# Kernel optimization log

Hardware: AMD Instinct MI355X
Metric: run time of the kernel (lower is better)

Reference implementation:

```python
import jax, jax.numpy as jnp
import numpy as np

N = 100_000          # nodes
E = 1_600_000        # real edges (self-loops appended after)
HID = 32             # hidden_dim
RES = 5              # PersistenceImager resolution -> 5x5 image
SIGMA = 0.2          # gaussian bandwidth of persistence image kernel
PRELU_A = 0.1        # F.prelu weight used in the source


def _linear_init(k, fan_in, fan_out):
    k1, k2 = jax.random.split(k)
    s = 1.0 / np.sqrt(fan_in)
    W = jax.random.uniform(k1, (fan_in, fan_out), minval=-s, maxval=s, dtype=jnp.float32)
    b = jax.random.uniform(k2, (fan_out,), minval=-s, maxval=s, dtype=jnp.float32)
    return W, b


def setup_inputs() -> dict:
    key = jax.random.key(0)
    ks = jax.random.split(key, 10)
    # edge list: E random edges, then N self-loops appended at the END
    src = jax.random.randint(ks[0], (E,), 0, N)
    dst = jax.random.randint(ks[1], (E,), 0, N)
    loops = jnp.arange(N)
    edge_index0 = jnp.stack([jnp.concatenate([src, loops]),
                             jnp.concatenate([dst, loops])]).astype(jnp.int64)
    x0 = jax.random.normal(ks[2], (N, 1), dtype=jnp.float32)
    # GIN conv MLPs (Base_Model with out_dim=hidden_dim)
    W1, b1 = _linear_init(ks[3], 1, HID)
    W2, b2 = _linear_init(ks[4], HID, HID)
    W4, b4 = _linear_init(ks[5], HID, HID)
    W3, b3 = _linear_init(ks[6], HID, HID)   # conv3: Linear only, no ReLU
    W5, b5 = _linear_init(ks[7], 2 * HID, HID)  # lin5
    W6, b6 = _linear_init(ks[8], HID, 2)        # lin6
    return dict(x0=x0, edge_index0=edge_index0,
                W1=W1, b1=b1, W2=W2, b2=b2, W4=W4, b4=b4, W3=W3, b3=b3,
                W5=W5, b5=b5, W6=W6, b6=b6)


def _gin_agg(x, src, dst):
    # PyG GINConv with eps=0: (1+eps)*x + sum_{j->i} x_j  (aggregation over the
    # provided edge_index, which here already includes appended self-loops)
    return x + jax.ops.segment_sum(x[src], dst, num_segments=N)


def _prelu(x):
    return jnp.where(x >= 0, x, PRELU_A * x)


def _pers_image(pd):
    # Persistence image on a RESxRES grid over [0,1]^2 of (birth, persistence),
    # gaussian kernel integrated per pixel via normal CDFs, linear pers weight.
    b = pd[:, 0]
    pers = pd[:, 1] - pd[:, 0]
    edges = jnp.linspace(0.0, 1.0, RES + 1)
    inv = 1.0 / (SIGMA * np.sqrt(2.0))
    cdf_b = 0.5 * (1.0 + jax.lax.erf((edges[None, :] - b[:, None]) * inv))   # [E, RES+1]
    cdf_p = 0.5 * (1.0 + jax.lax.erf((edges[None, :] - pers[:, None]) * inv))
    db = cdf_b[:, 1:] - cdf_b[:, :-1]   # [E, RES]
    dp = cdf_p[:, 1:] - cdf_p[:, :-1]
    img = jnp.einsum('e,ei,ej->ij', pers, db, dp)
    return img.reshape(-1)  # [25]


def reference(x0, edge_index0, W1, b1, W2, b2, W4, b4, W3, b3, W5, b5, W6, b6):
    src, dst = edge_index0[0], edge_index0[1]
    # Base_Model GIN path (dropout is identity in eval mode); order 1,2,4,3
    x = jax.nn.relu(_gin_agg(x0, src, dst) @ W1 + b1)
    x = jax.nn.relu(_gin_agg(x, src, dst) @ W2 + b2)
    x = jax.nn.relu(_gin_agg(x, src, dst) @ W4 + b4)
    x = _gin_agg(x, src, dst) @ W3 + b3      # conv3: Linear, no ReLU
    # edge head over the E real edges (drop trailing N self-loops)
    x_in = x[src[:E]]
    x_out = x[dst[:E]]
    h = _prelu(jnp.concatenate([x_in, x_out], axis=-1) @ W5 + b5)
    pd = h @ W6 + b6                          # predicted PD, [E, 2]
    img = _pers_image(pd)                     # persistence image, [25]
    return pd, img
```

## Files before the change

kernel.cpp:

```cpp
#include <hip/hip_runtime.h>
#include <hip/hip_bf16.h>
#include <hip/hip_fp16.h>
#include <math.h>

#define NN 100000
#define EE 1600000
#define ET 1700000
#define HID 32

#define BKT_SHIFT 10
#define BKT_MASK 1023
#define NBKT 98
#define CAP 18944
#define EPB 4096
#define NBLK_A 416
#define NBI 1024

__global__ __launch_bounds__(128) void k_seed(int* __restrict__ bucket_fill) {
    int t = threadIdx.x;
    if (t < NBKT) bucket_fill[t] = t * CAP;
}

__global__ __launch_bounds__(256) void k_bkt_scatter(const int* __restrict__ src32, const int* __restrict__ dst32,
                                                     int* __restrict__ bucket_fill, int2* __restrict__ pairs) {
    __shared__ int h[NBKT];
    __shared__ int bbase[NBKT];
    for (int i = threadIdx.x; i < NBKT; i += 256) h[i] = 0;
    __syncthreads();
    int base = blockIdx.x * EPB;
    for (int k = 0; k < EPB; k += 256) {
        int t = base + k + threadIdx.x;
        if (t < ET) atomicAdd(&h[dst32[t] >> BKT_SHIFT], 1);
    }
    __syncthreads();
    for (int i = threadIdx.x; i < NBKT; i += 256) {
        int c = h[i];
        bbase[i] = c ? atomicAdd(&bucket_fill[i], c) : 0;
        h[i] = 0;
    }
    __syncthreads();
    for (int k = 0; k < EPB; k += 256) {
        int t = base + k + threadIdx.x;
        if (t < ET) {
            int sv = src32[t], dv = dst32[t];
            int b = dv >> BKT_SHIFT;
            int off = atomicAdd(&h[b], 1);
            pairs[bbase[b] + off] = make_int2(sv, dv);
        }
    }
}

__global__ __launch_bounds__(512) void k_bkt_csr(const int2* __restrict__ pairs, const int* __restrict__ bucket_fill,
                                                 int* __restrict__ rowptr, int* __restrict__ rowend,
                                                 int* __restrict__ src_sorted) {
    __shared__ int h[1024];
    __shared__ int tmp[512];
    int t = threadIdx.x;
    int b = blockIdx.x;
    int e0 = b * CAP, e1 = bucket_fill[b];
    int node0 = b << BKT_SHIFT;

    h[t] = 0;
    h[t + 512] = 0;
    __syncthreads();
    for (int e = e0 + t; e < e1; e += 512) atomicAdd(&h[pairs[e].y & BKT_MASK], 1);
    __syncthreads();

    int i0 = 2 * t, i1 = 2 * t + 1;
    int v0 = h[i0], v1 = h[i1];
    int s = v0 + v1;
    tmp[t] = s;
    for (int off = 1; off < 512; off <<= 1) {
        __syncthreads();
        int u = (t >= off) ? tmp[t - off] : 0;
        __syncthreads();
        tmp[t] += u;
    }
    __syncthreads();
    int excl = tmp[t] - s;
    h[i0] = excl;
    h[i1] = excl + v0;
    __syncthreads();

    int n0 = node0 + i0, n1 = node0 + i1;
    if (n0 < NN) { rowptr[n0] = e0 + excl;      rowend[n0] = e0 + excl + v0; }
    if (n1 < NN) { rowptr[n1] = e0 + excl + v0; rowend[n1] = e0 + excl + v0 + v1; }
    __syncthreads();

    for (int e = e0 + t; e < e1; e += 512) {
        int2 p = pairs[e];
        int sl = atomicAdd(&h[p.y & BKT_MASK], 1);
        src_sorted[e0 + sl] = p.x;
    }
}

__device__ __forceinline__ void acc8(uint4 r, float* c) {
    float2 f0 = __half22float2(*reinterpret_cast<__half2*>(&r.x));
    float2 f1 = __half22float2(*reinterpret_cast<__half2*>(&r.y));
    float2 f2 = __half22float2(*reinterpret_cast<__half2*>(&r.z));
    float2 f3 = __half22float2(*reinterpret_cast<__half2*>(&r.w));
    c[0] += f0.x; c[1] += f0.y; c[2] += f1.x; c[3] += f1.y;
    c[4] += f2.x; c[5] += f2.y; c[6] += f3.x; c[7] += f3.y;
}

__global__ __launch_bounds__(256) void k_pull1(const int* __restrict__ rowptr, const int* __restrict__ rowend,
                                               const int* __restrict__ src_sorted,
                                               const float* __restrict__ x0, const float* __restrict__ W1,
                                               const float* __restrict__ b1, __half* __restrict__ hout) {
    __shared__ float W1l[32], b1l[32];
    if (threadIdx.x < 32) {
        W1l[threadIdx.x] = W1[threadIdx.x];
        b1l[threadIdx.x] = b1[threadIdx.x];
    }
    __syncthreads();
    int g = blockIdx.x * 256 + threadIdx.x;
    if (g >= NN) return;
    int e0 = rowptr[g], e1 = rowend[g];
    float a0 = x0[g], a1 = 0.f, a2 = 0.f, a3 = 0.f, a4 = 0.f, a5 = 0.f, a6 = 0.f, a7 = 0.f;
    int e = e0;
    for (; e + 8 <= e1; e += 8) {
        a0 += x0[src_sorted[e + 0]];
        a1 += x0[src_sorted[e + 1]];
        a2 += x0[src_sorted[e + 2]];
        a3 += x0[src_sorted[e + 3]];
        a4 += x0[src_sorted[e + 4]];
        a5 += x0[src_sorted[e + 5]];
        a6 += x0[src_sorted[e + 6]];
        a7 += x0[src_sorted[e + 7]];
    }
    for (; e < e1; ++e) a0 += x0[src_sorted[e]];
    float s = ((a0 + a1) + (a2 + a3)) + ((a4 + a5) + (a6 + a7));

    uint4* orow = reinterpret_cast<uint4*>(hout) + ((size_t)g << 2);
#pragma unroll
    for (int q = 0; q < 4; ++q) {
        float o0 = fmaxf(fmaf(s, W1l[8 * q + 0], b1l[8 * q + 0]), 0.f);
        float o1 = fmaxf(fmaf(s, W1l[8 * q + 1], b1l[8 * q + 1]), 0.f);
        float o2 = fmaxf(fmaf(s, W1l[8 * q + 2], b1l[8 * q + 2]), 0.f);
        float o3 = fmaxf(fmaf(s, W1l[8 * q + 3], b1l[8 * q + 3]), 0.f);
        float o4 = fmaxf(fmaf(s, W1l[8 * q + 4], b1l[8 * q + 4]), 0.f);
        float o5 = fmaxf(fmaf(s, W1l[8 * q + 5], b1l[8 * q + 5]), 0.f);
        float o6 = fmaxf(fmaf(s, W1l[8 * q + 6], b1l[8 * q + 6]), 0.f);
        float o7 = fmaxf(fmaf(s, W1l[8 * q + 7], b1l[8 * q + 7]), 0.f);
        __half2 p0 = __floats2half2_rn(o0, o1);
        __half2 p1 = __floats2half2_rn(o2, o3);
        __half2 p2 = __floats2half2_rn(o4, o5);
        __half2 p3 = __floats2half2_rn(o6, o7);
        orow[q] = make_uint4(*reinterpret_cast<unsigned*>(&p0), *reinterpret_cast<unsigned*>(&p1),
                             *reinterpret_cast<unsigned*>(&p2), *reinterpret_cast<unsigned*>(&p3));
    }
}

template <int RELU>
__global__ __launch_bounds__(256) void k_agg_mm(const int* __restrict__ rowptr, const int* __restrict__ rowend,
                                                const int* __restrict__ src_sorted,
                                                const __half* __restrict__ hin, const float* __restrict__ W,
                                                const float* __restrict__ b, __half* __restrict__ hout) {
    __shared__ float Wl[1024];
    for (int i = threadIdx.x; i < 1024; i += 256) Wl[i] = W[i];
    __syncthreads();
    int g = (blockIdx.x * 256 + threadIdx.x) >> 2;
    if (g >= NN) return;
    int j = threadIdx.x & 3;
    const uint4* tab = reinterpret_cast<const uint4*>(hin);
    int e0 = rowptr[g], e1 = rowend[g];
    float x[8], y[8];
#pragma unroll
    for (int i = 0; i < 8; ++i) { x[i] = 0.f; y[i] = 0.f; }
    acc8(tab[(g << 2) + j], x);
    int e = e0;
    for (; e + 8 <= e1; e += 8) {
        int s0 = src_sorted[e + 0], s1 = src_sorted[e + 1], s2 = src_sorted[e + 2], s3 = src_sorted[e + 3];
        int s4 = src_sorted[e + 4], s5 = src_sorted[e + 5], s6 = src_sorted[e + 6], s7 = src_sorted[e + 7];
        uint4 r0 = tab[(s0 << 2) + j];
        uint4 r1 = tab[(s1 << 2) + j];
        uint4 r2 = tab[(s2 << 2) + j];
        uint4 r3 = tab[(s3 << 2) + j];
        uint4 r4 = tab[(s4 << 2) + j];
        uint4 r5 = tab[(s5 << 2) + j];
        uint4 r6 = tab[(s6 << 2) + j];
        uint4 r7 = tab[(s7 << 2) + j];
        acc8(r0, x); acc8(r1, y); acc8(r2, x); acc8(r3, y);
        acc8(r4, x); acc8(r5, y); acc8(r6, x); acc8(r7, y);
    }
    for (; e < e1; ++e) acc8(tab[(src_sorted[e] << 2) + j], x);
#pragma unroll
    for (int i = 0; i < 8; ++i) x[i] += y[i];

    float o[8];
#pragma unroll
    for (int i = 0; i < 8; ++i) o[i] = b[8 * j + i];
#pragma unroll
    for (int sl = 0; sl < 4; ++sl) {
#pragma unroll
        for (int r = 0; r < 8; ++r) {
            float xk = __shfl(x[r], sl, 4);
            int k = 8 * sl + r;
            float4 w0 = *reinterpret_cast<const float4*>(&Wl[k * 32 + 8 * j]);
            float4 w1 = *reinterpret_cast<const float4*>(&Wl[k * 32 + 8 * j + 4]);
            o[0] = fmaf(xk, w0.x, o[0]); o[1] = fmaf(xk, w0.y, o[1]);
            o[2] = fmaf(xk, w0.z, o[2]); o[3] = fmaf(xk, w0.w, o[3]);
            o[4] = fmaf(xk, w1.x, o[4]); o[5] = fmaf(xk, w1.y, o[5]);
            o[6] = fmaf(xk, w1.z, o[6]); o[7] = fmaf(xk, w1.w, o[7]);
        }
    }
    if (RELU) {
#pragma unroll
        for (int i = 0; i < 8; ++i) o[i] = fmaxf(o[i], 0.f);
    }
    __half2 p0 = __floats2half2_rn(o[0], o[1]);
    __half2 p1 = __floats2half2_rn(o[2], o[3]);
    __half2 p2 = __floats2half2_rn(o[4], o[5]);
    __half2 p3 = __floats2half2_rn(o[6], o[7]);
    uint4 st = make_uint4(*reinterpret_cast<unsigned*>(&p0), *reinterpret_cast<unsigned*>(&p1),
                          *reinterpret_cast<unsigned*>(&p2), *reinterpret_cast<unsigned*>(&p3));
    reinterpret_cast<uint4*>(hout)[(g << 2) + j] = st;
}

__global__ __launch_bounds__(256) void k_agg_mm_proj(const int* __restrict__ rowptr, const int* __restrict__ rowend,
                                                     const int* __restrict__ src_sorted,
                                                     const __half* __restrict__ hin, const float* __restrict__ W3,
                                                     const float* __restrict__ b3,
                                                     const float* __restrict__ W5, const float* __restrict__ b5,
                                                     __half* __restrict__ u16, __half* __restrict__ v16) {
    __shared__ float W3l[1024];
    __shared__ float W5l[2048];
    for (int i = threadIdx.x; i < 1024; i += 256) W3l[i] = W3[i];
    for (int i = threadIdx.x; i < 2048; i += 256) W5l[i] = W5[i];
    __syncthreads();
    int g = (blockIdx.x * 256 + threadIdx.x) >> 2;
    if (g >= NN) return;
    int j = threadIdx.x & 3;
    const uint4* tab = reinterpret_cast<const uint4*>(hin);
    int e0 = rowptr[g], e1 = rowend[g];
    float x[8], y[8];
#pragma unroll
    for (int i = 0; i < 8; ++i) { x[i] = 0.f; y[i] = 0.f; }
    acc8(tab[(g << 2) + j], x);
    int e = e0;
    for (; e + 8 <= e1; e += 8) {
        int s0 = src_sorted[e + 0], s1 = src_sorted[e + 1], s2 = src_sorted[e + 2], s3 = src_sorted[e + 3];
        int s4 = src_sorted[e + 4], s5 = src_sorted[e + 5], s6 = src_sorted[e + 6], s7 = src_sorted[e + 7];
        uint4 r0 = tab[(s0 << 2) + j];
        uint4 r1 = tab[(s1 << 2) + j];
        uint4 r2 = tab[(s2 << 2) + j];
        uint4 r3 = tab[(s3 << 2) + j];
        uint4 r4 = tab[(s4 << 2) + j];
        uint4 r5 = tab[(s5 << 2) + j];
        uint4 r6 = tab[(s6 << 2) + j];
        uint4 r7 = tab[(s7 << 2) + j];
        acc8(r0, x); acc8(r1, y); acc8(r2, x); acc8(r3, y);
        acc8(r4, x); acc8(r5, y); acc8(r6, x); acc8(r7, y);
    }
    for (; e < e1; ++e) acc8(tab[(src_sorted[e] << 2) + j], x);
#pragma unroll
    for (int i = 0; i < 8; ++i) x[i] += y[i];

    float o[8];
#pragma unroll
    for (int i = 0; i < 8; ++i) o[i] = b3[8 * j + i];
#pragma unroll
    for (int sl = 0; sl < 4; ++sl) {
#pragma unroll
        for (int r = 0; r < 8; ++r) {
            float xk = __shfl(x[r], sl, 4);
            int k = 8 * sl + r;
            float4 w0 = *reinterpret_cast<const float4*>(&W3l[k * 32 + 8 * j]);
            float4 w1 = *reinterpret_cast<const float4*>(&W3l[k * 32 + 8 * j + 4]);
            o[0] = fmaf(xk, w0.x, o[0]); o[1] = fmaf(xk, w0.y, o[1]);
            o[2] = fmaf(xk, w0.z, o[2]); o[3] = fmaf(xk, w0.w, o[3]);
            o[4] = fmaf(xk, w1.x, o[4]); o[5] = fmaf(xk, w1.y, o[5]);
            o[6] = fmaf(xk, w1.z, o[6]); o[7] = fmaf(xk, w1.w, o[7]);
        }
    }
    float u[8], v[8];
#pragma unroll
    for (int i = 0; i < 8; ++i) { u[i] = b5[8 * j + i]; v[i] = 0.f; }
#pragma unroll
    for (int sl = 0; sl < 4; ++sl) {
#pragma unroll
        for (int r = 0; r < 8; ++r) {
            float xk = __shfl(o[r], sl, 4);
            int k = 8 * sl + r;
            float4 a0 = *reinterpret_cast<const float4*>(&W5l[k * 32 + 8 * j]);
            float4 a1 = *reinterpret_cast<const float4*>(&W5l[k * 32 + 8 * j + 4]);
            u[0] = fmaf(xk, a0.x, u[0]); u[1] = fmaf(xk, a0.y, u[1]);
            u[2] = fmaf(xk, a0.z, u[2]); u[3] = fmaf(xk, a0.w, u[3]);
            u[4] = fmaf(xk, a1.x, u[4]); u[5] = fmaf(xk, a1.y, u[5]);
            u[6] = fmaf(xk, a1.z, u[6]); u[7] = fmaf(xk, a1.w, u[7]);
            float4 c0 = *reinterpret_cast<const float4*>(&W5l[(32 + k) * 32 + 8 * j]);
            float4 c1 = *reinterpret_cast<const float4*>(&W5l[(32 + k) * 32 + 8 * j + 4]);
            v[0] = fmaf(xk, c0.x, v[0]); v[1] = fmaf(xk, c0.y, v[1]);
            v[2] = fmaf(xk, c0.z, v[2]); v[3] = fmaf(xk, c0.w, v[3]);
            v[4] = fmaf(xk, c1.x, v[4]); v[5] = fmaf(xk, c1.y, v[5]);
            v[6] = fmaf(xk, c1.z, v[6]); v[7] = fmaf(xk, c1.w, v[7]);
        }
    }
    __half2 pu0 = __floats2half2_rn(u[0], u[1]);
    __half2 pu1 = __floats2half2_rn(u[2], u[3]);
    __half2 pu2 = __floats2half2_rn(u[4], u[5]);
    __half2 pu3 = __floats2half2_rn(u[6], u[7]);
    uint4 su = make_uint4(*reinterpret_cast<unsigned*>(&pu0), *reinterpret_cast<unsigned*>(&pu1),
                          *reinterpret_cast<unsigned*>(&pu2), *reinterpret_cast<unsigned*>(&pu3));
    reinterpret_cast<uint4*>(u16)[(g << 2) + j] = su;
    __half2 pv0 = __floats2half2_rn(v[0], v[1]);
    __half2 pv1 = __floats2half2_rn(v[2], v[3]);
    __half2 pv2 = __floats2half2_rn(v[4], v[5]);
    __half2 pv3 = __floats2half2_rn(v[6], v[7]);
    uint4 sv = make_uint4(*reinterpret_cast<unsigned*>(&pv0), *reinterpret_cast<unsigned*>(&pv1),
                          *reinterpret_cast<unsigned*>(&pv2), *reinterpret_cast<unsigned*>(&pv3));
    reinterpret_cast<uint4*>(v16)[(g << 2) + j] = sv;
}

__global__ __launch_bounds__(256) void k_edge(const int* __restrict__ src32, const int* __restrict__ dst32,
                                              const __half* __restrict__ u16, const __half* __restrict__ v16,
                                              const float* __restrict__ W6, const float* __restrict__ b6,
                                              float* __restrict__ pd_out) {
    int ea = blockIdx.x * 512 + threadIdx.x;
    int eb = ea + 256;
    int sa = src32[ea], da = dst32[ea];
    int sb = src32[eb], db = dst32[eb];
    const uint4* pua = reinterpret_cast<const uint4*>(u16 + ((size_t)sa << 5));
    const uint4* pva = reinterpret_cast<const uint4*>(v16 + ((size_t)da << 5));
    const uint4* pub = reinterpret_cast<const uint4*>(u16 + ((size_t)sb << 5));
    const uint4* pvb = reinterpret_cast<const uint4*>(v16 + ((size_t)db << 5));

    uint4 A[4], B[4], C[4], D[4];
#pragma unroll
    for (int q = 0; q < 4; ++q) A[q] = pua[q];
#pragma unroll
    for (int q = 0; q < 4; ++q) B[q] = pva[q];
#pragma unroll
    for (int q = 0; q < 4; ++q) C[q] = pub[q];
#pragma unroll
    for (int q = 0; q < 4; ++q) D[q] = pvb[q];
    __builtin_amdgcn_sched_barrier(0);

    float b60 = b6[0], b61 = b6[1];
    float pda0 = b60, pda1 = b61, pdb0 = b60, pdb1 = b61;
#pragma unroll
    for (int q = 0; q < 4; ++q) {
        const __half2* ah = reinterpret_cast<const __half2*>(&A[q]);
        const __half2* bh = reinterpret_cast<const __half2*>(&B[q]);
        const __half2* ch = reinterpret_cast<const __half2*>(&C[q]);
        const __half2* dh = reinterpret_cast<const __half2*>(&D[q]);
#pragma unroll
        for (int r = 0; r < 4; ++r) {
            float2 fA = __half22float2(__hadd2(ah[r], bh[r]));
            float2 fB = __half22float2(__hadd2(ch[r], dh[r]));
            int jj = q * 8 + 2 * r;
            float w00 = W6[2 * jj + 0], w01 = W6[2 * jj + 1];
            float w10 = W6[2 * (jj + 1) + 0], w11 = W6[2 * (jj + 1) + 1];
            float hA0 = fA.x >= 0.f ? fA.x : 0.1f * fA.x;
            float hA1 = fA.y >= 0.f ? fA.y : 0.1f * fA.y;
            float hB0 = fB.x >= 0.f ? fB.x : 0.1f * fB.x;
            float hB1 = fB.y >= 0.f ? fB.y : 0.1f * fB.y;
            pda0 = fmaf(hA0, w00, pda0); pda1 = fmaf(hA0, w01, pda1);
            pda0 = fmaf(hA1, w10, pda0); pda1 = fmaf(hA1, w11, pda1);
            pdb0 = fmaf(hB0, w00, pdb0); pdb1 = fmaf(hB0, w01, pdb1);
            pdb0 = fmaf(hB1, w10, pdb0); pdb1 = fmaf(hB1, w11, pdb1);
        }
    }
    reinterpret_cast<float2*>(pd_out)[ea] = make_float2(pda0, pda1);
    reinterpret_cast<float2*>(pd_out)[eb] = make_float2(pdb0, pdb1);
}

__global__ __launch_bounds__(256) void k_pimg(const float* __restrict__ pd, float* __restrict__ partial) {
    float acc[25];
#pragma unroll
    for (int i = 0; i < 25; ++i) acc[i] = 0.f;
    const float inv = 3.5355339059327378f;

    for (int e = blockIdx.x * 256 + threadIdx.x; e < EE; e += NBI * 256) {
        float2 p = reinterpret_cast<const float2*>(pd)[e];
        float pers = p.y - p.x;
        float cb[6], cp[6];
#pragma unroll
        for (int i = 0; i < 6; ++i) {
            float te = 0.2f * (float)i;
            cb[i] = erff((te - p.x) * inv);
            cp[i] = erff((te - pers) * inv);
        }
#pragma unroll
        for (int i = 0; i < 5; ++i) {
            float pdb = 0.25f * pers * (cb[i + 1] - cb[i]);
#pragma unroll
            for (int jj = 0; jj < 5; ++jj)
                acc[i * 5 + jj] = fmaf(pdb, cp[jj + 1] - cp[jj], acc[i * 5 + jj]);
        }
    }

    int lane = threadIdx.x & 63;
    int wv = threadIdx.x >> 6;
    __shared__ float sacc[4][25];
#pragma unroll
    for (int i = 0; i < 25; ++i) {
        float v = acc[i];
        v += __shfl_down(v, 32);
        v += __shfl_down(v, 16);
        v += __shfl_down(v, 8);
        v += __shfl_down(v, 4);
        v += __shfl_down(v, 2);
        v += __shfl_down(v, 1);
        if (lane == 0) sacc[wv][i] = v;
    }
    __syncthreads();
    if (threadIdx.x < 25) {
        partial[(size_t)blockIdx.x * 25 + threadIdx.x] =
            sacc[0][threadIdx.x] + sacc[1][threadIdx.x] + sacc[2][threadIdx.x] + sacc[3][threadIdx.x];
    }
}

__global__ __launch_bounds__(256) void k_img(const float* __restrict__ partial, float* __restrict__ img) {
    int bin = blockIdx.x;
    float s = 0.f;
    for (int k = threadIdx.x; k < NBI; k += 256) s += partial[(size_t)k * 25 + bin];
    s += __shfl_down(s, 32);
    s += __shfl_down(s, 16);
    s += __shfl_down(s, 8);
    s += __shfl_down(s, 4);
    s += __shfl_down(s, 2);
    s += __shfl_down(s, 1);
    __shared__ float wsum[4];
    if ((threadIdx.x & 63) == 0) wsum[threadIdx.x >> 6] = s;
    __syncthreads();
    if (threadIdx.x == 0) img[bin] = wsum[0] + wsum[1] + wsum[2] + wsum[3];
}

extern "C" void kernel_launch(void* const* d_in, const int* in_sizes, int n_in,
                              void* d_out, int out_size, void* d_ws, size_t ws_size,
                              hipStream_t stream) {
    const float* x0 = (const float*)d_in[0];
    const int* src32 = (const int*)d_in[1];
    const int* dst32 = src32 + ET;
    const float* W1 = (const float*)d_in[2];
    const float* b1 = (const float*)d_in[3];
    const float* W2 = (const float*)d_in[4];
    const float* b2 = (const float*)d_in[5];
    const float* W4 = (const float*)d_in[6];
    const float* b4 = (const float*)d_in[7];
    const float* W3 = (const float*)d_in[8];
    const float* b3 = (const float*)d_in[9];
    const float* W5 = (const float*)d_in[10];
    const float* b5 = (const float*)d_in[11];
    const float* W6 = (const float*)d_in[12];
    const float* b6 = (const float*)d_in[13];
    float* out = (float*)d_out;

    const size_t PADDED = (size_t)NBKT * CAP;
    char* w = (char*)d_ws;
    int2* pairs = (int2*)w;
    int* src_sorted = (int*)(pairs + PADDED);
    int* bucket_fill = src_sorted + PADDED;
    int* rowptr = bucket_fill + NBKT;
    int* rowend = rowptr + NN;
    size_t off = ((size_t)((char*)(rowend + NN) - w) + 63) & ~(size_t)63;
    __half* bufA = (__half*)(w + off);
    __half* bufB = bufA + (size_t)NN * 32;
    __half* u16 = bufB + (size_t)NN * 32;
    __half* v16 = u16 + (size_t)NN * 32;
    float* partial = (float*)(v16 + (size_t)NN * 32);

    k_seed<<<1, 128, 0, stream>>>(bucket_fill);
    k_bkt_scatter<<<NBLK_A, 256, 0, stream>>>(src32, dst32, bucket_fill, pairs);
    k_bkt_csr<<<NBKT, 512, 0, stream>>>(pairs, bucket_fill, rowptr, rowend, src_sorted);

    k_pull1<<<(NN + 255) / 256, 256, 0, stream>>>(rowptr, rowend, src_sorted, x0, W1, b1, bufA);
    k_agg_mm<1><<<(NN * 4 + 255) / 256, 256, 0, stream>>>(rowptr, rowend, src_sorted, bufA, W2, b2, bufB);
    k_agg_mm<1><<<(NN * 4 + 255) / 256, 256, 0, stream>>>(rowptr, rowend, src_sorted, bufB, W4, b4, bufA);
    k_agg_mm_proj<<<(NN * 4 + 255) / 256, 256, 0, stream>>>(rowptr, rowend, src_sorted, bufA, W3, b3, W5, b5, u16, v16);

    k_edge<<<EE / 512, 256, 0, stream>>>(src32, dst32, u16, v16, W6, b6, out);
    k_pimg<<<NBI, 256, 0, stream>>>(out, partial);
    k_img<<<25, 256, 0, stream>>>(partial, out + 2 * (size_t)EE);
}
```

Measured before the change: 239.8 us.

## Pad CSR rows to multiples of eight and pack edge pairs into one int

After: 226.5 us. -5.5%, faster.

```diff
diff --git a/kernel.cpp b/kernel.cpp
--- a/kernel.cpp
+++ b/kernel.cpp
@@ -11,18 +11,30 @@
 #define BKT_SHIFT 10
 #define BKT_MASK 1023
 #define NBKT 98
-#define CAP 18944
+#define CAP 24576
 #define EPB 4096
 #define NBLK_A 416
 #define NBI 1024
 
-__global__ __launch_bounds__(128) void k_seed(int* __restrict__ bucket_fill) {
+__global__ __launch_bounds__(128) void k_seed(int* __restrict__ bucket_fill,
+                                              __half* __restrict__ bufA, __half* __restrict__ bufB) {
     int t = threadIdx.x;
     if (t < NBKT) bucket_fill[t] = t * CAP;
+    if (t >= 96) {
+        int i = t - 96;
+        bufA[(size_t)NN * 32 + i] = __float2half(0.f);
+        bufB[(size_t)NN * 32 + i] = __float2half(0.f);
+    }
+}
+
+__global__ __launch_bounds__(256) void k_xpad(const float* __restrict__ x0, float* __restrict__ x0p) {
+    int t = blockIdx.x * 256 + threadIdx.x;
+    if (t < NN) x0p[t] = x0[t];
+    if (t == NN) x0p[NN] = 0.f;
 }
 
 __global__ __launch_bounds__(256) void k_bkt_scatter(const int* __restrict__ src32, const int* __restrict__ dst32,
-                                                     int* __restrict__ bucket_fill, int2* __restrict__ pairs) {
+                                                     int* __restrict__ bucket_fill, int* __restrict__ packed) {
     __shared__ int h[NBKT];
     __shared__ int bbase[NBKT];
     for (int i = threadIdx.x; i < NBKT; i += 256) h[i] = 0;
@@ -45,15 +57,16 @@
             int sv = src32[t], dv = dst32[t];
             int b = dv >> BKT_SHIFT;
             int off = atomicAdd(&h[b], 1);
-            pairs[bbase[b] + off] = make_int2(sv, dv);
-        }
-    }
-}
-
-__global__ __launch_bounds__(512) void k_bkt_csr(const int2* __restrict__ pairs, const int* __restrict__ bucket_fill,
+            packed[bbase[b] + off] = (sv << 10) | (dv & BKT_MASK);
+        }
+    }
+}
+
+__global__ __launch_bounds__(512) void k_bkt_csr(const int* __restrict__ packed, const int* __restrict__ bucket_fill,
                                                  int* __restrict__ rowptr, int* __restrict__ rowend,
                                                  int* __restrict__ src_sorted) {
     __shared__ int h[1024];
+    __shared__ int pend[1024];
     __shared__ int tmp[512];
     int t = threadIdx.x;
     int b = blockIdx.x;
@@ -63,12 +76,14 @@
     h[t] = 0;
     h[t + 512] = 0;
     __syncthreads();
-    for (int e = e0 + t; e < e1; e += 512) atomicAdd(&h[pairs[e].y & BKT_MASK], 1);
+    for (int e = e0 + t; e < e1; e += 512) atomicAdd(&h[packed[e] & BKT_MASK], 1);
     __syncthreads();
 
     int i0 = 2 * t, i1 = 2 * t + 1;
     int v0 = h[i0], v1 = h[i1];
-    int s = v0 + v1;
+    int p0 = (v0 + 7) & ~7;
+    int p1 = (v1 + 7) & ~7;
+    int s = p0 + p1;
     tmp[t] = s;
     for (int off = 1; off < 512; off <<= 1) {
         __syncthreads();
@@ -79,18 +94,27 @@
     __syncthreads();
     int excl = tmp[t] - s;
     h[i0] = excl;
-    h[i1] = excl + v0;
+    h[i1] = excl + p0;
+    pend[i0] = excl + p0;
+    pend[i1] = excl + p0 + p1;
     __syncthreads();
 
     int n0 = node0 + i0, n1 = node0 + i1;
-    if (n0 < NN) { rowptr[n0] = e0 + excl;      rowend[n0] = e0 + excl + v0; }
-    if (n1 < NN) { rowptr[n1] = e0 + excl + v0; rowend[n1] = e0 + excl + v0 + v1; }
+    if (n0 < NN) { rowptr[n0] = e0 + h[i0]; rowend[n0] = e0 + pend[i0]; }
+    if (n1 < NN) { rowptr[n1] = e0 + h[i1]; rowend[n1] = e0 + pend[i1]; }
     __syncthreads();
 
     for (int e = e0 + t; e < e1; e += 512) {
-        int2 p = pairs[e];
-        int sl = atomicAdd(&h[p.y & BKT_MASK], 1);
-        src_sorted[e0 + sl] = p.x;
+        int pk = packed[e];
+        int sl = atomicAdd(&h[pk & BKT_MASK], 1);
+        src_sorted[e0 + sl] = pk >> 10;
+    }
+    __syncthreads();
+
+    for (int i = t; i < 1024; i += 512) {
+        if (node0 + i < NN) {
+            for (int e = h[i]; e < pend[i]; ++e) src_sorted[e0 + e] = NN;
+        }
     }
 }
 
@@ -105,7 +129,7 @@
 
 __global__ __launch_bounds__(256) void k_pull1(const int* __restrict__ rowptr, const int* __restrict__ rowend,
                                                const int* __restrict__ src_sorted,
-                                               const float* __restrict__ x0, const float* __restrict__ W1,
+                                               const float* __restrict__ x0p, const float* __restrict__ W1,
                                                const float* __restrict__ b1, __half* __restrict__ hout) {
     __shared__ float W1l[32], b1l[32];
     if (threadIdx.x < 32) {
@@ -116,19 +140,17 @@
     int g = blockIdx.x * 256 + threadIdx.x;
     if (g >= NN) return;
     int e0 = rowptr[g], e1 = rowend[g];
-    float a0 = x0[g], a1 = 0.f, a2 = 0.f, a3 = 0.f, a4 = 0.f, a5 = 0.f, a6 = 0.f, a7 = 0.f;
-    int e = e0;
-    for (; e + 8 <= e1; e += 8) {
-        a0 += x0[src_sorted[e + 0]];
-        a1 += x0[src_sorted[e + 1]];
-        a2 += x0[src_sorted[e + 2]];
-        a3 += x0[src_sorted[e + 3]];
-        a4 += x0[src_sorted[e + 4]];
-        a5 += x0[src_sorted[e + 5]];
-        a6 += x0[src_sorted[e + 6]];
-        a7 += x0[src_sorted[e + 7]];
-    }
-    for (; e < e1; ++e) a0 += x0[src_sorted[e]];
+    float a0 = x0p[g], a1 = 0.f, a2 = 0.f, a3 = 0.f, a4 = 0.f, a5 = 0.f, a6 = 0.f, a7 = 0.f;
+    for (int e = e0; e < e1; e += 8) {
+        a0 += x0p[src_sorted[e + 0]];
+        a1 += x0p[src_sorted[e + 1]];
+        a2 += x0p[src_sorted[e + 2]];
+        a3 += x0p[src_sorted[e + 3]];
+        a4 += x0p[src_sorted[e + 4]];
+        a5 += x0p[src_sorted[e + 5]];
+        a6 += x0p[src_sorted[e + 6]];
+        a7 += x0p[src_sorted[e + 7]];
+    }
     float s = ((a0 + a1) + (a2 + a3)) + ((a4 + a5) + (a6 + a7));
 
     uint4* orow = reinterpret_cast<uint4*>(hout) + ((size_t)g << 2);
@@ -151,6 +173,23 @@
     }
 }
 
+#define LOAD8(RR, EBASE)                                            \
+    {                                                               \
+        int s0 = src_sorted[(EBASE) + 0], s1 = src_sorted[(EBASE) + 1]; \
+        int s2 = src_sorted[(EBASE) + 2], s3 = src_sorted[(EBASE) + 3]; \
+        int s4 = src_sorted[(EBASE) + 4], s5 = src_sorted[(EBASE) + 5]; \
+        int s6 = src_sorted[(EBASE) + 6], s7 = src_sorted[(EBASE) + 7]; \
+        RR[0] = tab[(s0 << 2) + j]; RR[1] = tab[(s1 << 2) + j];     \
+        RR[2] = tab[(s2 << 2) + j]; RR[3] = tab[(s3 << 2) + j];     \
+        RR[4] = tab[(s4 << 2) + j]; RR[5] = tab[(s5 << 2) + j];     \
+        RR[6] = tab[(s6 << 2) + j]; RR[7] = tab[(s7 << 2) + j];     \
+    }
+#define CONS8(RR)                                                   \
+    {                                                               \
+        acc8(RR[0], x); acc8(RR[1], y); acc8(RR[2], x); acc8(RR[3], y); \
+        acc8(RR[4], x); acc8(RR[5], y); acc8(RR[6], x); acc8(RR[7], y); \
+    }
+
 template <int RELU>
 __global__ __launch_bounds__(256) void k_agg_mm(const int* __restrict__ rowptr, const int* __restrict__ rowend,
                                                 const int* __restrict__ src_sorted,
@@ -163,27 +202,24 @@
     if (g >= NN) return;
     int j = threadIdx.x & 3;
     const uint4* tab = reinterpret_cast<const uint4*>(hin);
-    int e0 = rowptr[g], e1 = rowend[g];
+    int e = rowptr[g], e1 = rowend[g];
     float x[8], y[8];
 #pragma unroll
     for (int i = 0; i < 8; ++i) { x[i] = 0.f; y[i] = 0.f; }
     acc8(tab[(g << 2) + j], x);
-    int e = e0;
-    for (; e + 8 <= e1; e += 8) {
-        int s0 = src_sorted[e + 0], s1 = src_sorted[e + 1], s2 = src_sorted[e + 2], s3 = src_sorted[e + 3];
-        int s4 = src_sorted[e + 4], s5 = src_sorted[e + 5], s6 = src_sorted[e + 6], s7 = src_sorted[e + 7];
-        uint4 r0 = tab[(s0 << 2) + j];
-        uint4 r1 = tab[(s1 << 2) + j];
-        uint4 r2 = tab[(s2 << 2) + j];
-        uint4 r3 = tab[(s3 << 2) + j];
-        uint4 r4 = tab[(s4 << 2) + j];
-        uint4 r5 = tab[(s5 << 2) + j];
-        uint4 r6 = tab[(s6 << 2) + j];
-        uint4 r7 = tab[(s7 << 2) + j];
-        acc8(r0, x); acc8(r1, y); acc8(r2, x); acc8(r3, y);
-        acc8(r4, x); acc8(r5, y); acc8(r6, x); acc8(r7, y);
-    }
-    for (; e < e1; ++e) acc8(tab[(src_sorted[e] << 2) + j], x);
+    uint4 rA[8], rB[8];
+    for (; e + 16 <= e1; e += 16) {
+        LOAD8(rA, e)
+        LOAD8(rB, e + 8)
+        __builtin_amdgcn_sched_barrier(0);
+        CONS8(rA)
+        CONS8(rB)
+    }
+    if (e < e1) {
+        LOAD8(rA, e)
+        __builtin_amdgcn_sched_barrier(0);
+        CONS8(rA)
+    }
 #pragma unroll
     for (int i = 0; i < 8; ++i) x[i] += y[i];
 
@@ -232,27 +268,24 @@
     if (g >= NN) return;
     int j = threadIdx.x & 3;
     const uint4* tab = reinterpret_cast<const uint4*>(hin);
-    int e0 = rowptr[g], e1 = rowend[g];
+    int e = rowptr[g], e1 = rowend[g];
     float x[8], y[8];
 #pragma unroll
     for (int i = 0; i < 8; ++i) { x[i] = 0.f; y[i] = 0.f; }
     acc8(tab[(g << 2) + j], x);
-    int e = e0;
-    for (; e + 8 <= e1; e += 8) {
-        int s0 = src_sorted[e + 0], s1 = src_sorted[e + 1], s2 = src_sorted[e + 2], s3 = src_sorted[e + 3];
-        int s4 = src_sorted[e + 4], s5 = src_sorted[e + 5], s6 = src_sorted[e + 6], s7 = src_sorted[e + 7];
-        uint4 r0 = tab[(s0 << 2) + j];
-        uint4 r1 = tab[(s1 << 2) + j];
-        uint4 r2 = tab[(s2 << 2) + j];
-        uint4 r3 = tab[(s3 << 2) + j];
-        uint4 r4 = tab[(s4 << 2) + j];
-        uint4 r5 = tab[(s5 << 2) + j];
-        uint4 r6 = tab[(s6 << 2) + j];
-        uint4 r7 = tab[(s7 << 2) + j];
-        acc8(r0, x); acc8(r1, y); acc8(r2, x); acc8(r3, y);
-        acc8(r4, x); acc8(r5, y); acc8(r6, x); acc8(r7, y);
-    }
-    for (; e < e1; ++e) acc8(tab[(src_sorted[e] << 2) + j], x);
+    uint4 rA[8], rB[8];
+    for (; e + 16 <= e1; e += 16) {
+        LOAD8(rA, e)
+        LOAD8(rB, e + 8)
+        __builtin_amdgcn_sched_barrier(0);
+        CONS8(rA)
+        CONS8(rB)
+    }
+    if (e < e1) {
+        LOAD8(rA, e)
+        __builtin_amdgcn_sched_barrier(0);
+        CONS8(rA)
+    }
 #pragma unroll
     for (int i = 0; i < 8; ++i) x[i] += y[i];
 
@@ -449,23 +482,25 @@
 
     const size_t PADDED = (size_t)NBKT * CAP;
     char* w = (char*)d_ws;
-    int2* pairs = (int2*)w;
-    int* src_sorted = (int*)(pairs + PADDED);
+    int* packed = (int*)w;
+    int* src_sorted = packed + PADDED;
     int* bucket_fill = src_sorted + PADDED;
     int* rowptr = bucket_fill + NBKT;
     int* rowend = rowptr + NN;
-    size_t off = ((size_t)((char*)(rowend + NN) - w) + 63) & ~(size_t)63;
+    float* x0p = (float*)(rowend + NN);
+    size_t off = ((size_t)((char*)(x0p + NN + 1) - w) + 63) & ~(size_t)63;
     __half* bufA = (__half*)(w + off);
-    __half* bufB = bufA + (size_t)NN * 32;
-    __half* u16 = bufB + (size_t)NN * 32;
+    __half* bufB = bufA + (size_t)(NN + 1) * 32;
+    __half* u16 = bufB + (size_t)(NN + 1) * 32;
     __half* v16 = u16 + (size_t)NN * 32;
     float* partial = (float*)(v16 + (size_t)NN * 32);
 
-    k_seed<<<1, 128, 0, stream>>>(bucket_fill);
-    k_bkt_scatter<<<NBLK_A, 256, 0, stream>>>(src32, dst32, bucket_fill, pairs);
-    k_bkt_csr<<<NBKT, 512, 0, stream>>>(pairs, bucket_fill, rowptr, rowend, src_sorted);
-
-    k_pull1<<<(NN + 255) / 256, 256, 0, stream>>>(rowptr, rowend, src_sorted, x0, W1, b1, bufA);
+    k_seed<<<1, 128, 0, stream>>>(bucket_fill, bufA, bufB);
+    k_xpad<<<(NN + 256) / 256, 256, 0, stream>>>(x0, x0p);
+    k_bkt_scatter<<<NBLK_A, 256, 0, stream>>>(src32, dst32, bucket_fill, packed);
+    k_bkt_csr<<<NBKT, 512, 0, stream>>>(packed, bucket_fill, rowptr, rowend, src_sorted);
+
+    k_pull1<<<(NN + 255) / 256, 256, 0, stream>>>(rowptr, rowend, src_sorted, x0p, W1, b1, bufA);
     k_agg_mm<1><<<(NN * 4 + 255) / 256, 256, 0, stream>>>(rowptr, rowend, src_sorted, bufA, W2, b2, bufB);
     k_agg_mm<1><<<(NN * 4 + 255) / 256, 256, 0, stream>>>(rowptr, rowend, src_sorted, bufB, W4, b4, bufA);
     k_agg_mm_proj<<<(NN * 4 + 255) / 256, 256, 0, stream>>>(rowptr, rowend, src_sorted, bufA, W3, b3, W5, b5, u16, v16);
```
